# Performance work log

Hardware: AMD Instinct MI355X
Metric: run time of the kernel (lower is better)

Reference implementation:

```python
import jax, jax.numpy as jnp
import numpy as np

C = 64


def setup_inputs() -> dict:
    key = jax.random.key(0)
    ks = jax.random.split(key, 7)
    x = jax.random.normal(ks[0], (8, C, 64, 64), dtype=jnp.float32)
    # 1x1 conv weights stored as [out_c, in_c]; biases [out_c]
    s = 1.0 / np.sqrt(C)
    W1 = jax.random.uniform(ks[1], (C, C), jnp.float32, -s, s)
    b1 = jax.random.uniform(ks[2], (C,), jnp.float32, -s, s)
    W2 = jax.random.uniform(ks[3], (C, C), jnp.float32, -s, s)
    b2 = jax.random.uniform(ks[4], (C,), jnp.float32, -s, s)
    W3 = jax.random.uniform(ks[5], (C, C), jnp.float32, -s, s)
    b3 = jax.random.uniform(ks[6], (C,), jnp.float32, -s, s)
    return {"x": x, "W1": W1, "b1": b1, "W2": W2, "b2": b2, "W3": W3, "b3": b3}


def reference(x, W1, b1, W2, b2, W3, b3):
    gamma = 1.0
    b, c, h, w = x.shape
    xf = x.reshape(b, c, h * w)  # [b, c, n]
    # 1x1 convs == per-pixel channel matmuls
    f = jnp.einsum('oc,bcn->bon', W1, xf) + b1[None, :, None]
    g = jnp.einsum('oc,bcn->bon', W2, xf) + b2[None, :, None]
    k = jnp.einsum('oc,bcn->bon', W3, xf) + b3[None, :, None]
    # scores[b,i,j] = sum_c f[b,c,i] * g[b,c,j]; softmax over j
    scores = jnp.einsum('bci,bcj->bij', f, g)
    attn = jax.nn.softmax(scores, axis=2)
    # out_attn[b,c,i] = sum_j attn[b,i,j] * k[b,c,j]
    out = jnp.einsum('bij,bcj->bci', attn, k).reshape(b, c, h, w)
    return gamma * out + x
```

## Files before the change

kernel.cpp:

```cpp
#include <hip/hip_runtime.h>
#include <hip/hip_bf16.h>

#define NPIX 4096
#define CCH  64
#define NB   8
#define KVBLK 64

typedef __attribute__((ext_vector_type(8)))  short short8;
typedef __attribute__((ext_vector_type(4)))  float f32x4;
typedef __attribute__((ext_vector_type(16))) float f32x16;

#define LOG2E   1.44269504f

__global__ __launch_bounds__(256) void proj_kernel(
    const float* __restrict__ x,
    const float* __restrict__ W1, const float* __restrict__ b1,
    const float* __restrict__ W2, const float* __restrict__ b2,
    const float* __restrict__ W3, const float* __restrict__ b3,
    __hip_bfloat16* __restrict__ Q, __hip_bfloat16* __restrict__ G,
    __hip_bfloat16* __restrict__ K)
{
    const int m    = blockIdx.x % 3;
    const int tile = blockIdx.x / 3;
    const int b    = tile >> 6;
    const int i0   = (tile & 63) << 6;

    const float* W  = (m == 0) ? W1 : (m == 1) ? W2 : W3;
    const float* bv = (m == 0) ? b1 : (m == 1) ? b2 : b3;

    __shared__ float xs[64][65];
    __shared__ float Wt[64][68];

    for (int e = threadIdx.x; e < 4096; e += 256) {
        const int c = e >> 6, p = e & 63;
        xs[c][p] = x[(size_t)b * CCH * NPIX + (size_t)c * NPIX + i0 + p];
        Wt[e & 63][e >> 6] = W[e];
    }
    __syncthreads();

    const int p = threadIdx.x & 63;
    const int g = threadIdx.x >> 6;

    float acc[16];
    #pragma unroll
    for (int oo = 0; oo < 16; ++oo) acc[oo] = bv[g * 16 + oo];

    for (int c = 0; c < 64; ++c) {
        const float xv = xs[c][p];
        const f32x4* w = (const f32x4*)&Wt[c][g * 16];
        #pragma unroll
        for (int qq = 0; qq < 4; ++qq) {
            const f32x4 a = w[qq];
            #pragma unroll
            for (int j = 0; j < 4; ++j)
                acc[qq * 4 + j] += a[j] * xv;
        }
    }

    const int i = i0 + p;
    if (m == 0) {
        #pragma unroll
        for (int oo = 0; oo < 16; ++oo)
            Q[(size_t)b * NPIX * CCH + (size_t)i * CCH + g * 16 + oo] =
                __float2bfloat16(acc[oo] * LOG2E);
    } else if (m == 1) {
        #pragma unroll
        for (int oo = 0; oo < 16; ++oo)
            G[(size_t)b * NPIX * CCH + (size_t)i * CCH + g * 16 + oo] =
                __float2bfloat16(acc[oo]);
    } else {
        #pragma unroll
        for (int oo = 0; oo < 16; ++oo)
            K[(size_t)b * CCH * NPIX + (size_t)(g * 16 + oo) * NPIX + i] =
                __float2bfloat16(acc[oo]);
    }
}

__device__ __forceinline__ void gload_lds16(const void* g, void* l) {
    __builtin_amdgcn_global_load_lds(
        (const __attribute__((address_space(1))) unsigned int*)g,
        (__attribute__((address_space(3))) unsigned int*)l, 16, 0, 0);
}
__device__ __forceinline__ unsigned int pack_bf16(float lo, float hi) {
    union { __hip_bfloat162 h; unsigned int u; } w;
    w.h = __float22bfloat162_rn(make_float2(lo, hi));
    return w.u;
}

__global__ __launch_bounds__(512, 4) void attn_kernel(
    const __hip_bfloat16* __restrict__ Qg, const __hip_bfloat16* __restrict__ Gg,
    const __hip_bfloat16* __restrict__ Kg,
    __hip_bfloat16* __restrict__ Opart, float* __restrict__ Lpart, int split)
{
    __shared__ char lds[2][16384];

    const int blk   = blockIdx.x;
    const int per_b = 16 * split;
    const int b     = blk / per_b;
    const int rem   = blk - b * per_b;
    const int itile = rem / split;
    const int sp    = rem - itile * split;
    const int tid   = threadIdx.x;
    const int wave  = tid >> 6;
    const int lane  = tid & 63;
    const int l32   = lane & 31;
    const int hi    = lane >> 5;
    const int i0w   = itile * 256 + wave * 32;
    const int jcnt  = NPIX / split;
    const int jlo   = sp * jcnt;
    const int niter = jcnt / KVBLK;

    const short* Qb = (const short*)Qg + (size_t)b * NPIX * CCH;
    const char*  Gb = (const char*)(Gg + (size_t)b * NPIX * CCH);
    const char*  Kb = (const char*)(Kg + (size_t)b * CCH * NPIX);

    short8 q[4];
    #pragma unroll
    for (int ks = 0; ks < 4; ++ks)
        q[ks] = *(const short8*)(Qb + (size_t)(i0w + l32) * CCH + ks * 16 + hi * 8);

    int gbase[2], kbase[2];
    #pragma unroll
    for (int jb = 0; jb < 2; ++jb)
        gbase[jb] = (jb * 32 + l32) * 128 + ((l32 & 7) << 4);
    #pragma unroll
    for (int cb = 0; cb < 2; ++cb)
        kbase[cb] = 8192 + (cb * 32 + l32) * 128 + ((l32 & 7) << 4);

    const int srow = tid >> 3, scolb = (tid & 7) * 16;
    const char* gsrc = Gb + (size_t)(jlo + srow) * 128 + (scolb ^ ((srow & 7) << 4));
    const char* ksrc = Kb + (size_t)srow * 8192 + (size_t)jlo * 2 + (scolb ^ ((srow & 7) << 4));

    f32x16 zacc;
    #pragma unroll
    for (int r = 0; r < 16; ++r) zacc[r] = 0.f;

    f32x16 o[2];
    #pragma unroll
    for (int cb = 0; cb < 2; ++cb)
        #pragma unroll
        for (int r = 0; r < 16; ++r) o[cb][r] = 0.f;
    float ps = 0.f;

    auto STAGE = [&](int buf, int tt) {
        gload_lds16(gsrc + tt * (KVBLK * 128), lds[buf] + wave * 1024);
        gload_lds16(ksrc + tt * (KVBLK * 2),  lds[buf] + 8192 + wave * 1024);
    };

    STAGE(0, 0);
    __syncthreads();

    for (int t = 0; t < niter; ++t) {
        const int cur = t & 1;
        STAGE(cur ^ 1, (t + 1 < niter) ? t + 1 : 0);
        const char* L = lds[cur];

        #pragma unroll
        for (int jb = 0; jb < 2; ++jb) {
            short8 ga[4];
            #pragma unroll
            for (int ks = 0; ks < 4; ++ks)
                ga[ks] = *(const short8*)(L + (gbase[jb] ^ ((2 * ks + hi) << 4)));

            __builtin_amdgcn_s_setprio(1);
            f32x16 acc = __builtin_amdgcn_mfma_f32_32x32x16_bf16(ga[0], q[0], zacc, 0, 0, 0);
            acc = __builtin_amdgcn_mfma_f32_32x32x16_bf16(ga[1], q[1], acc, 0, 0, 0);
            acc = __builtin_amdgcn_mfma_f32_32x32x16_bf16(ga[2], q[2], acc, 0, 0, 0);
            acc = __builtin_amdgcn_mfma_f32_32x32x16_bf16(ga[3], q[3], acc, 0, 0, 0);
            __builtin_amdgcn_s_setprio(0);

            float p[16];
            #pragma unroll
            for (int r = 0; r < 16; ++r) {
                p[r] = __builtin_amdgcn_exp2f(acc[r]);
                ps += p[r];
            }
            short8 pf[2];
            #pragma unroll
            for (int kk = 0; kk < 2; ++kk) {
                unsigned int x0 = pack_bf16(p[8 * kk + 0], p[8 * kk + 1]);
                unsigned int x1 = pack_bf16(p[8 * kk + 2], p[8 * kk + 3]);
                unsigned int y0 = pack_bf16(p[8 * kk + 4], p[8 * kk + 5]);
                unsigned int y1 = pack_bf16(p[8 * kk + 6], p[8 * kk + 7]);
                asm("v_permlane32_swap_b32 %0, %1" : "+v"(x0), "+v"(y0));
                asm("v_permlane32_swap_b32 %0, %1" : "+v"(x1), "+v"(y1));
                union { unsigned int u[4]; short8 v; } w;
                w.u[0] = x0; w.u[1] = x1; w.u[2] = y0; w.u[3] = y1;
                pf[kk] = w.v;
            }

            __builtin_amdgcn_s_setprio(1);
            #pragma unroll
            for (int kk = 0; kk < 2; ++kk) {
                const int ksg = 2 * jb + kk;
                const short8 ka0 = *(const short8*)(L + (kbase[0] ^ ((2 * ksg + hi) << 4)));
                const short8 ka1 = *(const short8*)(L + (kbase[1] ^ ((2 * ksg + hi) << 4)));
                o[0] = __builtin_amdgcn_mfma_f32_32x32x16_bf16(ka0, pf[kk], o[0], 0, 0, 0);
                o[1] = __builtin_amdgcn_mfma_f32_32x32x16_bf16(ka1, pf[kk], o[1], 0, 0, 0);
            }
            __builtin_amdgcn_s_setprio(0);
        }
        __syncthreads();
    }

    const size_t pb = (size_t)(b * split + sp);
    #pragma unroll
    for (int cb = 0; cb < 2; ++cb)
        #pragma unroll
        for (int r = 0; r < 16; ++r) {
            const int c = cb * 32 + (r & 3) + 8 * (r >> 2) + 4 * hi;
            const int i = i0w + l32;
            Opart[(pb * CCH + c) * NPIX + i] = __float2bfloat16(o[cb][r]);
        }
    ps += __shfl_xor(ps, 32);
    if (lane < 32)
        Lpart[pb * NPIX + i0w + l32] = ps;
}

__global__ __launch_bounds__(256) void combine_kernel(
    const __hip_bfloat16* __restrict__ Opart, const float* __restrict__ Lpart,
    const float* __restrict__ x, float* __restrict__ out, int split)
{
    const int b  = blockIdx.x >> 6;
    const int i0 = (blockIdx.x & 63) << 6;

    __shared__ float invL[64];
    if (threadIdx.x < 64) {
        const int i = i0 + threadIdx.x;
        float L = 0.f;
        for (int s = 0; s < split; ++s)
            L += Lpart[((size_t)(b * split + s)) * NPIX + i];
        invL[threadIdx.x] = 1.0f / L;
    }
    __syncthreads();

    const int c    = threadIdx.x >> 2;
    const int ioff = (threadIdx.x & 3) * 16;

    float acc[16];
    #pragma unroll
    for (int k = 0; k < 16; ++k) acc[k] = 0.f;

    for (int s = 0; s < split; ++s) {
        const size_t base = (((size_t)(b * split + s)) * CCH + c) * NPIX + i0 + ioff;
        const short8 v0 = *(const short8*)((const short*)Opart + base);
        const short8 v1 = *(const short8*)((const short*)Opart + base + 8);
        #pragma unroll
        for (int k = 0; k < 8; ++k) {
            union { unsigned int u; float f; } cv0, cv1;
            cv0.u = ((unsigned int)(unsigned short)v0[k]) << 16;
            cv1.u = ((unsigned int)(unsigned short)v1[k]) << 16;
            acc[k]     += cv0.f;
            acc[k + 8] += cv1.f;
        }
    }

    const size_t idx = ((size_t)b * CCH + c) * NPIX + i0 + ioff;
    #pragma unroll
    for (int kq = 0; kq < 4; ++kq) {
        const f32x4 xv = *(const f32x4*)&x[idx + 4 * kq];
        f32x4 r;
        #pragma unroll
        for (int t = 0; t < 4; ++t)
            r[t] = acc[kq * 4 + t] * invL[ioff + kq * 4 + t] + xv[t];
        *(f32x4*)&out[idx + 4 * kq] = r;
    }
}

extern "C" void kernel_launch(void* const* d_in, const int* in_sizes, int n_in,
                              void* d_out, int out_size, void* d_ws, size_t ws_size,
                              hipStream_t stream) {
    const float* x  = (const float*)d_in[0];
    const float* W1 = (const float*)d_in[1];
    const float* b1 = (const float*)d_in[2];
    const float* W2 = (const float*)d_in[3];
    const float* b2 = (const float*)d_in[4];
    const float* W3 = (const float*)d_in[5];
    const float* b3 = (const float*)d_in[6];
    float* out = (float*)d_out;

    char* ws = (char*)d_ws;
    const size_t planeB = (size_t)NB * NPIX * CCH * sizeof(__hip_bfloat16);
    __hip_bfloat16* Q = (__hip_bfloat16*)(ws);
    __hip_bfloat16* G = (__hip_bfloat16*)(ws + planeB);
    __hip_bfloat16* K = (__hip_bfloat16*)(ws + 2 * planeB);

    const size_t base   = 3 * planeB;
    const size_t oPlane = planeB;
    const size_t lPlane = (size_t)NB * NPIX * sizeof(float);

    int split = 8;
    while (split > 1 && base + (size_t)split * (oPlane + lPlane) > ws_size)
        split >>= 1;

    __hip_bfloat16* Opart = (__hip_bfloat16*)(ws + base);
    float* Lpart = (float*)(ws + base + (size_t)split * oPlane);

    proj_kernel<<<dim3(NB * 64 * 3), dim3(256), 0, stream>>>(x, W1, b1, W2, b2, W3, b3, Q, G, K);
    attn_kernel<<<dim3(NB * 16 * split), dim3(512), 0, stream>>>(Q, G, K, Opart, Lpart, split);
    combine_kernel<<<dim3(NB * 64), dim3(256), 0, stream>>>(Opart, Lpart, x, out, split);
}
```

Before: 82.94 us.

## Compute all three 1x1 projections per block with bf16 MFMA

The projection kernel now handles all three weight matrices in one block per 64-pixel tile, so the x tile is read once instead of three times. The scalar fp32 FMA loop is replaced by 32x32x16 bf16 MFMA instructions, with x and the weights converted to bf16 in LDS. This cuts redundant global loads of x and the ALU cost of the projection. In exchange, inputs to the projection are rounded to bf16 before accumulation, adding error, and the grid is three times smaller.

```diff
diff --git a/kernel.cpp b/kernel.cpp
--- a/kernel.cpp
+++ b/kernel.cpp
@@ -11,6 +11,12 @@
 typedef __attribute__((ext_vector_type(16))) float f32x16;
 
 #define LOG2E   1.44269504f
+
+__device__ __forceinline__ unsigned int pack_bf16(float lo, float hi) {
+    union { __hip_bfloat162 h; unsigned int u; } w;
+    w.h = __float22bfloat162_rn(make_float2(lo, hi));
+    return w.u;
+}
 
 __global__ __launch_bounds__(256) void proj_kernel(
     const float* __restrict__ x,
@@ -20,59 +26,81 @@
     __hip_bfloat16* __restrict__ Q, __hip_bfloat16* __restrict__ G,
     __hip_bfloat16* __restrict__ K)
 {
-    const int m    = blockIdx.x % 3;
-    const int tile = blockIdx.x / 3;
-    const int b    = tile >> 6;
-    const int i0   = (tile & 63) << 6;
-
-    const float* W  = (m == 0) ? W1 : (m == 1) ? W2 : W3;
-    const float* bv = (m == 0) ? b1 : (m == 1) ? b2 : b3;
-
-    __shared__ float xs[64][65];
-    __shared__ float Wt[64][68];
-
-    for (int e = threadIdx.x; e < 4096; e += 256) {
-        const int c = e >> 6, p = e & 63;
-        xs[c][p] = x[(size_t)b * CCH * NPIX + (size_t)c * NPIX + i0 + p];
-        Wt[e & 63][e >> 6] = W[e];
+    const int b    = blockIdx.x >> 6;
+    const int i0   = (blockIdx.x & 63) << 6;
+    const int tid  = threadIdx.x;
+    const int wave = tid >> 6;
+    const int lane = tid & 63;
+    const int l32  = lane & 31;
+    const int hi   = lane >> 5;
+
+    __shared__ __hip_bfloat16 Xt[64][72];
+    __shared__ __hip_bfloat16 Wb[3][64][64];
+    __shared__ float bsh[3][64];
+
+    for (int e = tid; e < 1024; e += 256) {
+        const int c = e >> 4, p4 = (e & 15) * 4;
+        const f32x4 v = *(const f32x4*)&x[((size_t)b * CCH + c) * NPIX + i0 + p4];
+        #pragma unroll
+        for (int t = 0; t < 4; ++t)
+            Xt[p4 + t][c] = __float2bfloat16(v[t]);
+    }
+    #pragma unroll
+    for (int m = 0; m < 3; ++m) {
+        const float* W = (m == 0) ? W1 : (m == 1) ? W2 : W3;
+        for (int e = tid; e < 1024; e += 256) {
+            const int oc = e >> 4, c4 = (e & 15) * 4;
+            const f32x4 v = *(const f32x4*)&W[oc * 64 + c4];
+            *(unsigned int*)&Wb[m][oc][c4]     = pack_bf16(v[0], v[1]);
+            *(unsigned int*)&Wb[m][oc][c4 + 2] = pack_bf16(v[2], v[3]);
+        }
+    }
+    if (tid < 192) {
+        const int m = tid >> 6, oc = tid & 63;
+        bsh[m][oc] = ((m == 0) ? b1 : (m == 1) ? b2 : b3)[oc];
     }
     __syncthreads();
 
-    const int p = threadIdx.x & 63;
-    const int g = threadIdx.x >> 6;
-
-    float acc[16];
-    #pragma unroll
-    for (int oo = 0; oo < 16; ++oo) acc[oo] = bv[g * 16 + oo];
-
-    for (int c = 0; c < 64; ++c) {
-        const float xv = xs[c][p];
-        const f32x4* w = (const f32x4*)&Wt[c][g * 16];
-        #pragma unroll
-        for (int qq = 0; qq < 4; ++qq) {
-            const f32x4 a = w[qq];
-            #pragma unroll
-            for (int j = 0; j < 4; ++j)
-                acc[qq * 4 + j] += a[j] * xv;
-        }
-    }
-
-    const int i = i0 + p;
-    if (m == 0) {
-        #pragma unroll
-        for (int oo = 0; oo < 16; ++oo)
-            Q[(size_t)b * NPIX * CCH + (size_t)i * CCH + g * 16 + oo] =
-                __float2bfloat16(acc[oo] * LOG2E);
-    } else if (m == 1) {
-        #pragma unroll
-        for (int oo = 0; oo < 16; ++oo)
-            G[(size_t)b * NPIX * CCH + (size_t)i * CCH + g * 16 + oo] =
-                __float2bfloat16(acc[oo]);
-    } else {
-        #pragma unroll
-        for (int oo = 0; oo < 16; ++oo)
-            K[(size_t)b * CCH * NPIX + (size_t)(g * 16 + oo) * NPIX + i] =
-                __float2bfloat16(acc[oo]);
+    #pragma unroll
+    for (int u = 0; u < 3; ++u) {
+        const int unit = wave + 4 * u;
+        const int m  = unit >> 2;
+        const int sr = (unit >> 1) & 1;
+        const int sc = unit & 1;
+
+        f32x16 acc;
+        #pragma unroll
+        for (int r = 0; r < 16; ++r) {
+            const int oc = sr * 32 + (r & 3) + 8 * (r >> 2) + 4 * hi;
+            acc[r] = bsh[m][oc];
+        }
+        #pragma unroll
+        for (int ks = 0; ks < 4; ++ks) {
+            const short8 af = *(const short8*)&Wb[m][sr * 32 + l32][ks * 16 + hi * 8];
+            const short8 bf = *(const short8*)&Xt[sc * 32 + l32][ks * 16 + hi * 8];
+            acc = __builtin_amdgcn_mfma_f32_32x32x16_bf16(af, bf, acc, 0, 0, 0);
+        }
+
+        const int i = i0 + sc * 32 + l32;
+        if (m == 0) {
+            #pragma unroll
+            for (int r = 0; r < 16; ++r) {
+                const int oc = sr * 32 + (r & 3) + 8 * (r >> 2) + 4 * hi;
+                Q[((size_t)b * NPIX + i) * CCH + oc] = __float2bfloat16(acc[r] * LOG2E);
+            }
+        } else if (m == 1) {
+            #pragma unroll
+            for (int r = 0; r < 16; ++r) {
+                const int oc = sr * 32 + (r & 3) + 8 * (r >> 2) + 4 * hi;
+                G[((size_t)b * NPIX + i) * CCH + oc] = __float2bfloat16(acc[r]);
+            }
+        } else {
+            #pragma unroll
+            for (int r = 0; r < 16; ++r) {
+                const int oc = sr * 32 + (r & 3) + 8 * (r >> 2) + 4 * hi;
+                K[((size_t)b * CCH + oc) * NPIX + i] = __float2bfloat16(acc[r]);
+            }
+        }
     }
 }
 
@@ -80,11 +108,6 @@
     __builtin_amdgcn_global_load_lds(
         (const __attribute__((address_space(1))) unsigned int*)g,
         (__attribute__((address_space(3))) unsigned int*)l, 16, 0, 0);
-}
-__device__ __forceinline__ unsigned int pack_bf16(float lo, float hi) {
-    union { __hip_bfloat162 h; unsigned int u; } w;
-    w.h = __float22bfloat162_rn(make_float2(lo, hi));
-    return w.u;
 }
 
 __global__ __launch_bounds__(512, 4) void attn_kernel(
@@ -296,7 +319,7 @@
     __hip_bfloat16* Opart = (__hip_bfloat16*)(ws + base);
     float* Lpart = (float*)(ws + base + (size_t)split * oPlane);
 
-    proj_kernel<<<dim3(NB * 64 * 3), dim3(256), 0, stream>>>(x, W1, b1, W2, b2, W3, b3, Q, G, K);
+    proj_kernel<<<dim3(NB * 64), dim3(256), 0, stream>>>(x, W1, b1, W2, b2, W3, b3, Q, G, K);
     attn_kernel<<<dim3(NB * 16 * split), dim3(512), 0, stream>>>(Q, G, K, Opart, Lpart, split);
     combine_kernel<<<dim3(NB * 64), dim3(256), 0, stream>>>(Opart, Lpart, x, out, split);
 }
```

Result: faster. 73.09 us, median of 2 (-11.9%).
